# Kernel tuning notes

Hardware: AMD Instinct MI355X
Metric: run time of the kernel (lower is better)

## Reference

```python
import jax, jax.numpy as jnp
import numpy as np

N = 65536
APP = 1024
SP = 512
HID = 512
CARD = 16
SUB = HID // CARD  # 32


def setup_inputs() -> dict:
    key = jax.random.key(0)
    ks = jax.random.split(key, 8)
    s1 = 1.0 / np.sqrt(APP)
    s2 = 1.0 / np.sqrt(SP)
    s3 = 1.0 / np.sqrt(SUB)
    return {
        "appearance": jax.random.normal(ks[0], (N, APP), jnp.float32),
        "spatial": jax.random.normal(ks[1], (N, SP), jnp.float32),
        # Batched per-branch weights (torch Linear: y = x @ W.T + b; here stored as [in, out])
        "W1": jax.random.uniform(ks[2], (CARD, APP, SUB), jnp.float32, -s1, s1),
        "b1": jax.random.uniform(ks[3], (CARD, SUB), jnp.float32, -s1, s1),
        "W2": jax.random.uniform(ks[4], (CARD, SP, SUB), jnp.float32, -s2, s2),
        "b2": jax.random.uniform(ks[5], (CARD, SP if False else SUB), jnp.float32, -s2, s2),
        "W3": jax.random.uniform(ks[6], (CARD, SUB, HID), jnp.float32, -s3, s3),
        "b3": jax.random.uniform(ks[7], (CARD, HID), jnp.float32, -s3, s3),
    }


def reference(appearance, spatial, W1, b1, W2, b2, W3, b3):
    # fc1[c] = appearance @ W1[c] + b1[c]; fc2[c] = spatial @ W2[c] + b2[c]
    h1 = jnp.einsum('na,cas->ncs', appearance, W1) + b1[None]  # [N, C, SUB]
    h2 = jnp.einsum('np,cps->ncs', spatial, W2) + b2[None]     # [N, C, SUB]
    h = jax.nn.relu(h1 + h2)
    # sum over branches of (h[:,c] @ W3[c] + b3[c]) == einsum + sum of biases
    out = jnp.einsum('ncs,csh->nh', h, W3) + jnp.sum(b3, axis=0)[None]  # [N, HID]
    return jax.nn.relu(out)
```

## Files before the change

kernel.cpp:

```cpp
#include <hip/hip_runtime.h>

typedef __attribute__((ext_vector_type(4))) float floatx4;
typedef __attribute__((ext_vector_type(8))) short bf16x8;

__device__ __forceinline__ unsigned short f2bf(float f) {
    union { float f; unsigned u; } v; v.f = f;
    unsigned r = v.u + 0x7fffu + ((v.u >> 16) & 1u);
    return (unsigned short)(r >> 16);
}

__global__ void prep_kernel(const float* __restrict__ W1, const float* __restrict__ b1,
                            const float* __restrict__ W2, const float* __restrict__ b2,
                            const float* __restrict__ W3, const float* __restrict__ b3,
                            unsigned short* __restrict__ wcat, unsigned short* __restrict__ w3f,
                            float* __restrict__ bias12, float* __restrict__ bias3s)
{
    int tid = blockIdx.x * 256 + threadIdx.x;
    if (tid < 98304) {
        int l  = tid & 63;
        int nt = (tid >> 6) & 31;
        int kc = tid >> 11;
        int n  = nt * 16 + (l & 15);
        int k0 = kc * 32 + ((l >> 4) << 3);
        int c = n >> 5, s = n & 31;
        union { unsigned short us[8]; int4 v; } pk;
        const float* src = (k0 < 1024) ? (W1 + c * 32768 + k0 * 32 + s)
                                       : (W2 + c * 16384 + (k0 - 1024) * 32 + s);
        #pragma unroll
        for (int j = 0; j < 8; ++j) pk.us[j] = f2bf(src[j * 32]);
        *(int4*)(wcat + (size_t)tid * 8) = pk.v;
    } else if (tid < 131072) {
        int t  = tid - 98304;
        int l  = t & 63;
        int nt = (t >> 6) & 31;
        int kc = t >> 11;
        int n  = nt * 16 + (l & 15);
        int k0 = kc * 32 + ((l >> 4) << 3);
        union { unsigned short us[8]; int4 v; } pk;
        const float* src = W3 + k0 * 512 + n;
        #pragma unroll
        for (int j = 0; j < 8; ++j) pk.us[j] = f2bf(src[j * 512]);
        *(int4*)(w3f + (size_t)t * 8) = pk.v;
    } else if (tid < 131584) {
        int n = tid - 131072;
        bias12[n] = b1[n] + b2[n];
        float sacc = 0.f;
        #pragma unroll
        for (int c = 0; c < 16; ++c) sacc += b3[c * 512 + n];
        bias3s[n] = sacc;
    }
}

__global__ __launch_bounds__(512, 4) void fused_main(
    const float* __restrict__ app, const float* __restrict__ sp,
    const unsigned short* __restrict__ wcat, const unsigned short* __restrict__ w3f,
    const float* __restrict__ bias12, const float* __restrict__ bias3s,
    float* __restrict__ out)
{
    __shared__ union {
        unsigned short As[2][2][4][64][8];
        unsigned short Hf[4][16][64][8];
    } sh;

    const int tid = (int)threadIdx.x;
    const int w   = tid >> 6;
    const int l   = tid & 63;
    const int rowbase = (int)blockIdx.x * 64;

    const int sr = tid >> 3;
    const int kq = tid & 7;
    const float* appsrc = app + (size_t)(rowbase + sr) * 1024 + kq * 8;
    const float* spsrc  = sp  + (size_t)(rowbase + sr) * 512  + kq * 8;

    const int halfw = kq >> 2, mtw = sr >> 4;
    const int Lw    = ((kq & 3) << 4) + (sr & 15);
    const int roww  = Lw >> 3, slotw = Lw & 7;
    const int wroff = halfw * 4096 + mtw * 1024 + roww * 128 + ((slotw ^ roww) << 4);
    char* shb = (char*)&sh;
    unsigned short* as0 = (unsigned short*)(shb + wroff);
    unsigned short* as1 = (unsigned short*)(shb + 8192 + wroff);

    const int rdoff = ((l >> 3) << 7) + (((l & 7) ^ (l >> 3)) << 4);
    #define AS_RD(buf, half, mt) \
        (*(const bf16x8*)(shb + (buf) * 8192 + (half) * 4096 + (mt) * 1024 + rdoff))

    floatx4 acc[4][4];
    #pragma unroll
    for (int mt = 0; mt < 4; ++mt)
        #pragma unroll
        for (int nt = 0; nt < 4; ++nt)
            acc[mt][nt] = (floatx4){0.f, 0.f, 0.f, 0.f};

    const unsigned short* wbase = wcat + (size_t)w * 2048 + (size_t)l * 8;

    bf16x8 bcur[8];
    #pragma unroll
    for (int i = 0; i < 8; ++i)
        bcur[i] = *(const bf16x8*)(wbase + (i >> 2) * 16384 + (i & 3) * 512);
    {
        float4 q0 = *(const float4*)(appsrc);
        float4 q1 = *(const float4*)(appsrc + 4);
        union { unsigned short us[8]; int4 v; } pk;
        pk.us[0] = f2bf(q0.x); pk.us[1] = f2bf(q0.y); pk.us[2] = f2bf(q0.z); pk.us[3] = f2bf(q0.w);
        pk.us[4] = f2bf(q1.x); pk.us[5] = f2bf(q1.y); pk.us[6] = f2bf(q1.z); pk.us[7] = f2bf(q1.w);
        *(int4*)as0 = pk.v;
    }
    float4 pA0 = *(const float4*)(appsrc + 64);
    float4 pA1 = *(const float4*)(appsrc + 68);
    asm volatile("s_waitcnt lgkmcnt(0)" ::: "memory");
    __builtin_amdgcn_s_barrier();

    for (int p = 0; p < 24; ++p) {
        const int buf = p & 1;

        if (p + 1 < 24) {
            union { unsigned short us[8]; int4 v; } pk;
            pk.us[0] = f2bf(pA0.x); pk.us[1] = f2bf(pA0.y); pk.us[2] = f2bf(pA0.z); pk.us[3] = f2bf(pA0.w);
            pk.us[4] = f2bf(pA1.x); pk.us[5] = f2bf(pA1.y); pk.us[6] = f2bf(pA1.z); pk.us[7] = f2bf(pA1.w);
            *(int4*)((buf == 0) ? as1 : as0) = pk.v;
        }

        bf16x8 af[4];
        #pragma unroll
        for (int mt = 0; mt < 4; ++mt)
            af[mt] = AS_RD(buf, 0, mt);
        __builtin_amdgcn_s_setprio(1);
        #pragma unroll
        for (int mt = 0; mt < 4; ++mt)
            #pragma unroll
            for (int nt = 0; nt < 4; ++nt)
                acc[mt][nt] = __builtin_amdgcn_mfma_f32_16x16x32_bf16(
                    af[mt], bcur[nt], acc[mt][nt], 0, 0, 0);
        __builtin_amdgcn_s_setprio(0);

        if (p + 2 < 24) {
            const int c = p + 2;
            const float* src = (c < 16) ? (appsrc + c * 64) : (spsrc + (c - 16) * 64);
            pA0 = *(const float4*)src;
            pA1 = *(const float4*)(src + 4);
        }

        #pragma unroll
        for (int mt = 0; mt < 4; ++mt)
            af[mt] = AS_RD(buf, 1, mt);
        __builtin_amdgcn_s_setprio(1);
        #pragma unroll
        for (int mt = 0; mt < 4; ++mt)
            #pragma unroll
            for (int nt = 0; nt < 4; ++nt)
                acc[mt][nt] = __builtin_amdgcn_mfma_f32_16x16x32_bf16(
                    af[mt], bcur[4 + nt], acc[mt][nt], 0, 0, 0);
        __builtin_amdgcn_s_setprio(0);

        if (p + 1 < 24) {
            const unsigned short* wp = wbase + (size_t)(p + 1) * 32768;
            #pragma unroll
            for (int i = 0; i < 8; ++i)
                bcur[i] = *(const bf16x8*)(wp + (i >> 2) * 16384 + (i & 3) * 512);
        }

        asm volatile("s_waitcnt lgkmcnt(0)" ::: "memory");
        __builtin_amdgcn_s_barrier();
    }

    const unsigned short* w3base = w3f + (size_t)w * 2048 + (size_t)l * 8;
    bf16x8 b3[8];
    #pragma unroll
    for (int i = 0; i < 8; ++i)
        b3[i] = *(const bf16x8*)(w3base + (i >> 2) * 16384 + (i & 3) * 512);

    #pragma unroll
    for (int nt = 0; nt < 4; ++nt) {
        const int colg = w * 64 + nt * 16 + (l & 15);
        const float bv = bias12[colg];
        const int kc  = colg >> 5;
        const int lhi = ((colg >> 3) & 3) << 4;
        const int j   = colg & 7;
        #pragma unroll
        for (int mt = 0; mt < 4; ++mt)
            #pragma unroll
            for (int r = 0; r < 4; ++r) {
                const int rlow = ((l >> 4) << 2) + r;
                float v = acc[mt][nt][r] + bv;
                v = fmaxf(v, 0.f);
                sh.Hf[mt][kc][lhi + rlow][j] = f2bf(v);
            }
    }
    asm volatile("s_waitcnt lgkmcnt(0)" ::: "memory");
    __builtin_amdgcn_s_barrier();

    #pragma unroll
    for (int mt = 0; mt < 4; ++mt)
        #pragma unroll
        for (int nt = 0; nt < 4; ++nt)
            acc[mt][nt] = (floatx4){0.f, 0.f, 0.f, 0.f};

    for (int q = 0; q < 8; ++q) {
        bf16x8 af[4];
        #pragma unroll
        for (int mt = 0; mt < 4; ++mt)
            af[mt] = *(const bf16x8*)(&sh.Hf[mt][2 * q][l][0]);
        __builtin_amdgcn_s_setprio(1);
        #pragma unroll
        for (int mt = 0; mt < 4; ++mt)
            #pragma unroll
            for (int nt = 0; nt < 4; ++nt)
                acc[mt][nt] = __builtin_amdgcn_mfma_f32_16x16x32_bf16(
                    af[mt], b3[nt], acc[mt][nt], 0, 0, 0);
        __builtin_amdgcn_s_setprio(0);
        #pragma unroll
        for (int mt = 0; mt < 4; ++mt)
            af[mt] = *(const bf16x8*)(&sh.Hf[mt][2 * q + 1][l][0]);
        __builtin_amdgcn_s_setprio(1);
        #pragma unroll
        for (int mt = 0; mt < 4; ++mt)
            #pragma unroll
            for (int nt = 0; nt < 4; ++nt)
                acc[mt][nt] = __builtin_amdgcn_mfma_f32_16x16x32_bf16(
                    af[mt], b3[4 + nt], acc[mt][nt], 0, 0, 0);
        __builtin_amdgcn_s_setprio(0);
        if (q + 1 < 8) {
            const unsigned short* wp = w3base + (size_t)(q + 1) * 32768;
            #pragma unroll
            for (int i = 0; i < 8; ++i)
                b3[i] = *(const bf16x8*)(wp + (i >> 2) * 16384 + (i & 3) * 512);
        }
    }

    #pragma unroll
    for (int nt = 0; nt < 4; ++nt) {
        const int colg = w * 64 + nt * 16 + (l & 15);
        const float bv = bias3s[colg];
        #pragma unroll
        for (int mt = 0; mt < 4; ++mt)
            #pragma unroll
            for (int r = 0; r < 4; ++r) {
                const int rowg = mt * 16 + ((l >> 4) << 2) + r;
                float v = acc[mt][nt][r] + bv;
                v = fmaxf(v, 0.f);
                out[(size_t)(rowbase + rowg) * 512 + colg] = v;
            }
    }
    #undef AS_RD
}

extern "C" void kernel_launch(void* const* d_in, const int* in_sizes, int n_in,
                              void* d_out, int out_size, void* d_ws, size_t ws_size,
                              hipStream_t stream)
{
    const float* app = (const float*)d_in[0];
    const float* sp  = (const float*)d_in[1];
    const float* W1  = (const float*)d_in[2];
    const float* b1  = (const float*)d_in[3];
    const float* W2  = (const float*)d_in[4];
    const float* b2  = (const float*)d_in[5];
    const float* W3  = (const float*)d_in[6];
    const float* b3  = (const float*)d_in[7];

    char* ws = (char*)d_ws;
    unsigned short* wcat  = (unsigned short*)(ws);
    unsigned short* w3f   = (unsigned short*)(ws + 1572864);
    float*          b12   = (float*)(ws + 2097152);
    float*          b3s   = (float*)(ws + 2099200);

    prep_kernel<<<514, 256, 0, stream>>>(W1, b1, W2, b2, W3, b3, wcat, w3f, b12, b3s);

    float* outp = (float*)d_out;
    fused_main<<<65536 / 64, 512, 0, stream>>>(app, sp, wcat, w3f, b12, b3s, outp);
}
```

Before: 551.0 us.

## Split K-step into half-phases with extra barriers to interleave LDS reads and MFMA

```diff
diff --git a/kernel.cpp b/kernel.cpp
--- a/kernel.cpp
+++ b/kernel.cpp
@@ -62,6 +62,9 @@
         unsigned short Hf[4][16][64][8];
     } sh;
 
+    #define BARRIER() asm volatile("s_barrier" ::: "memory")
+    #define LGKM0()   asm volatile("s_waitcnt lgkmcnt(0)" ::: "memory")
+
     const int tid = (int)threadIdx.x;
     const int w   = tid >> 6;
     const int l   = tid & 63;
@@ -93,10 +96,13 @@
 
     const unsigned short* wbase = wcat + (size_t)w * 2048 + (size_t)l * 8;
 
-    bf16x8 bcur[8];
-    #pragma unroll
-    for (int i = 0; i < 8; ++i)
-        bcur[i] = *(const bf16x8*)(wbase + (i >> 2) * 16384 + (i & 3) * 512);
+    bf16x8 bA[4], bB[4];
+    #pragma unroll
+    for (int i = 0; i < 4; ++i)
+        bA[i] = *(const bf16x8*)(wbase + i * 512);
+    #pragma unroll
+    for (int i = 0; i < 4; ++i)
+        bB[i] = *(const bf16x8*)(wbase + 16384 + i * 512);
     {
         float4 q0 = *(const float4*)(appsrc);
         float4 q1 = *(const float4*)(appsrc + 4);
@@ -107,67 +113,76 @@
     }
     float4 pA0 = *(const float4*)(appsrc + 64);
     float4 pA1 = *(const float4*)(appsrc + 68);
-    asm volatile("s_waitcnt lgkmcnt(0)" ::: "memory");
-    __builtin_amdgcn_s_barrier();
+    LGKM0();
+    BARRIER();
 
     for (int p = 0; p < 24; ++p) {
         const int buf = p & 1;
-
+        bf16x8 af[4];
+
+        #pragma unroll
+        for (int mt = 0; mt < 4; ++mt)
+            af[mt] = AS_RD(buf, 0, mt);
         if (p + 1 < 24) {
             union { unsigned short us[8]; int4 v; } pk;
             pk.us[0] = f2bf(pA0.x); pk.us[1] = f2bf(pA0.y); pk.us[2] = f2bf(pA0.z); pk.us[3] = f2bf(pA0.w);
             pk.us[4] = f2bf(pA1.x); pk.us[5] = f2bf(pA1.y); pk.us[6] = f2bf(pA1.z); pk.us[7] = f2bf(pA1.w);
             *(int4*)((buf == 0) ? as1 : as0) = pk.v;
         }
-
-        bf16x8 af[4];
-        #pragma unroll
-        for (int mt = 0; mt < 4; ++mt)
-            af[mt] = AS_RD(buf, 0, mt);
-        __builtin_amdgcn_s_setprio(1);
-        #pragma unroll
-        for (int mt = 0; mt < 4; ++mt)
-            #pragma unroll
-            for (int nt = 0; nt < 4; ++nt)
-                acc[mt][nt] = __builtin_amdgcn_mfma_f32_16x16x32_bf16(
-                    af[mt], bcur[nt], acc[mt][nt], 0, 0, 0);
-        __builtin_amdgcn_s_setprio(0);
-
         if (p + 2 < 24) {
             const int c = p + 2;
             const float* src = (c < 16) ? (appsrc + c * 64) : (spsrc + (c - 16) * 64);
             pA0 = *(const float4*)src;
             pA1 = *(const float4*)(src + 4);
         }
-
-        #pragma unroll
-        for (int mt = 0; mt < 4; ++mt)
-            af[mt] = AS_RD(buf, 1, mt);
-        __builtin_amdgcn_s_setprio(1);
-        #pragma unroll
-        for (int mt = 0; mt < 4; ++mt)
-            #pragma unroll
-            for (int nt = 0; nt < 4; ++nt)
-                acc[mt][nt] = __builtin_amdgcn_mfma_f32_16x16x32_bf16(
-                    af[mt], bcur[4 + nt], acc[mt][nt], 0, 0, 0);
-        __builtin_amdgcn_s_setprio(0);
-
+        BARRIER();
+        LGKM0();
+        __builtin_amdgcn_s_setprio(1);
+        #pragma unroll
+        for (int mt = 0; mt < 4; ++mt)
+            #pragma unroll
+            for (int nt = 0; nt < 4; ++nt)
+                acc[mt][nt] = __builtin_amdgcn_mfma_f32_16x16x32_bf16(
+                    af[mt], bA[nt], acc[mt][nt], 0, 0, 0);
+        __builtin_amdgcn_s_setprio(0);
         if (p + 1 < 24) {
             const unsigned short* wp = wbase + (size_t)(p + 1) * 32768;
             #pragma unroll
-            for (int i = 0; i < 8; ++i)
-                bcur[i] = *(const bf16x8*)(wp + (i >> 2) * 16384 + (i & 3) * 512);
-        }
-
-        asm volatile("s_waitcnt lgkmcnt(0)" ::: "memory");
-        __builtin_amdgcn_s_barrier();
+            for (int i = 0; i < 4; ++i)
+                bA[i] = *(const bf16x8*)(wp + i * 512);
+        }
+        BARRIER();
+
+        #pragma unroll
+        for (int mt = 0; mt < 4; ++mt)
+            af[mt] = AS_RD(buf, 1, mt);
+        BARRIER();
+        LGKM0();
+        __builtin_amdgcn_s_setprio(1);
+        #pragma unroll
+        for (int mt = 0; mt < 4; ++mt)
+            #pragma unroll
+            for (int nt = 0; nt < 4; ++nt)
+                acc[mt][nt] = __builtin_amdgcn_mfma_f32_16x16x32_bf16(
+                    af[mt], bB[nt], acc[mt][nt], 0, 0, 0);
+        __builtin_amdgcn_s_setprio(0);
+        if (p + 1 < 24) {
+            const unsigned short* wp = wbase + (size_t)(p + 1) * 32768;
+            #pragma unroll
+            for (int i = 0; i < 4; ++i)
+                bB[i] = *(const bf16x8*)(wp + 16384 + i * 512);
+        }
+        BARRIER();
     }
 
     const unsigned short* w3base = w3f + (size_t)w * 2048 + (size_t)l * 8;
-    bf16x8 b3[8];
-    #pragma unroll
-    for (int i = 0; i < 8; ++i)
-        b3[i] = *(const bf16x8*)(w3base + (i >> 2) * 16384 + (i & 3) * 512);
+    bf16x8 b3A[4], b3B[4];
+    #pragma unroll
+    for (int i = 0; i < 4; ++i)
+        b3A[i] = *(const bf16x8*)(w3base + i * 512);
+    #pragma unroll
+    for (int i = 0; i < 4; ++i)
+        b3B[i] = *(const bf16x8*)(w3base + 16384 + i * 512);
 
     #pragma unroll
     for (int nt = 0; nt < 4; ++nt) {
@@ -186,8 +201,8 @@
                 sh.Hf[mt][kc][lhi + rlow][j] = f2bf(v);
             }
     }
-    asm volatile("s_waitcnt lgkmcnt(0)" ::: "memory");
-    __builtin_amdgcn_s_barrier();
+    LGKM0();
+    BARRIER();
 
     #pragma unroll
     for (int mt = 0; mt < 4; ++mt)
@@ -200,31 +215,43 @@
         #pragma unroll
         for (int mt = 0; mt < 4; ++mt)
             af[mt] = *(const bf16x8*)(&sh.Hf[mt][2 * q][l][0]);
-        __builtin_amdgcn_s_setprio(1);
-        #pragma unroll
-        for (int mt = 0; mt < 4; ++mt)
-            #pragma unroll
-            for (int nt = 0; nt < 4; ++nt)
-                acc[mt][nt] = __builtin_amdgcn_mfma_f32_16x16x32_bf16(
-                    af[mt], b3[nt], acc[mt][nt], 0, 0, 0);
-        __builtin_amdgcn_s_setprio(0);
-        #pragma unroll
-        for (int mt = 0; mt < 4; ++mt)
-            af[mt] = *(const bf16x8*)(&sh.Hf[mt][2 * q + 1][l][0]);
-        __builtin_amdgcn_s_setprio(1);
-        #pragma unroll
-        for (int mt = 0; mt < 4; ++mt)
-            #pragma unroll
-            for (int nt = 0; nt < 4; ++nt)
-                acc[mt][nt] = __builtin_amdgcn_mfma_f32_16x16x32_bf16(
-                    af[mt], b3[4 + nt], acc[mt][nt], 0, 0, 0);
+        BARRIER();
+        LGKM0();
+        __builtin_amdgcn_s_setprio(1);
+        #pragma unroll
+        for (int mt = 0; mt < 4; ++mt)
+            #pragma unroll
+            for (int nt = 0; nt < 4; ++nt)
+                acc[mt][nt] = __builtin_amdgcn_mfma_f32_16x16x32_bf16(
+                    af[mt], b3A[nt], acc[mt][nt], 0, 0, 0);
         __builtin_amdgcn_s_setprio(0);
         if (q + 1 < 8) {
             const unsigned short* wp = w3base + (size_t)(q + 1) * 32768;
             #pragma unroll
-            for (int i = 0; i < 8; ++i)
-                b3[i] = *(const bf16x8*)(wp + (i >> 2) * 16384 + (i & 3) * 512);
-        }
+            for (int i = 0; i < 4; ++i)
+                b3A[i] = *(const bf16x8*)(wp + i * 512);
+        }
+        BARRIER();
+        #pragma unroll
+        for (int mt = 0; mt < 4; ++mt)
+            af[mt] = *(const bf16x8*)(&sh.Hf[mt][2 * q + 1][l][0]);
+        BARRIER();
+        LGKM0();
+        __builtin_amdgcn_s_setprio(1);
+        #pragma unroll
+        for (int mt = 0; mt < 4; ++mt)
+            #pragma unroll
+            for (int nt = 0; nt < 4; ++nt)
+                acc[mt][nt] = __builtin_amdgcn_mfma_f32_16x16x32_bf16(
+                    af[mt], b3B[nt], acc[mt][nt], 0, 0, 0);
+        __builtin_amdgcn_s_setprio(0);
+        if (q + 1 < 8) {
+            const unsigned short* wp = w3base + (size_t)(q + 1) * 32768;
+            #pragma unroll
+            for (int i = 0; i < 4; ++i)
+                b3B[i] = *(const bf16x8*)(wp + 16384 + i * 512);
+        }
+        BARRIER();
     }
 
     #pragma unroll
@@ -242,6 +269,8 @@
             }
     }
     #undef AS_RD
+    #undef BARRIER
+    #undef LGKM0
 }
 
 extern "C" void kernel_launch(void* const* d_in, const int* in_sizes, int n_in,
```

Result: slower. 597.9 us (+8.5%).
